# Performance work log

Measured on AMD Instinct MI355X. Metric: run time of the kernel, lower is better.

## Reference

```python
import jax, jax.numpy as jnp
import numpy as np

K = 7          # involution kernel size
GC = 16        # group_channels
BN_EPS = 1e-5


def conv1x1(x, w, b):
    # x: [b,c,h,w], w: [o,c], b: [o]
    return jnp.einsum('bchw,oc->bohw', x, w) + b[None, :, None, None]


def involution(x, w1, b1, w2, b2):
    # x: [b,c,h,w]; stride=1, kernel K, padding K//2
    b_, c, h, w = x.shape
    g = c // GC
    # per-pixel kernel weights: conv1x1 -> conv1x1 (no activation, as in source)
    wgt = conv1x1(conv1x1(x, w1, b1), w2, b2).reshape(b_, g, K * K, h, w)
    # patches: [b, c*K*K, h, w] with channel-major (c, kh, kw) ordering, matching torch Unfold
    pat = jax.lax.conv_general_dilated_patches(
        x, (K, K), (1, 1), ((K // 2, K // 2), (K // 2, K // 2)))
    pat = pat.reshape(b_, g, GC, K * K, h, w)
    out = jnp.einsum('bgkhw,bgckhw->bgchw', wgt, pat)
    return out.reshape(b_, c, h, w)


def hswish(x):
    return x * jnp.clip(x + 3.0, 0.0, 6.0) / 6.0


def setup_inputs() -> dict:
    key = jax.random.key(0)
    ks = jax.random.split(key, 20)
    inp, oup, mip = 256, 256, 64
    n, h, w = 16, 96, 96
    rr = 4  # involution reduction_ratio

    def rn(k, shape, s=0.05):
        return (jax.random.normal(k, shape) * s).astype(jnp.float32)

    def invp(k0, k1, k2, k3):
        return (rn(k0, (mip // rr, mip)), rn(k1, (mip // rr,)),
                rn(k2, (K * K * (mip // GC), mip // rr)),
                rn(k3, (K * K * (mip // GC),)))

    d = {}
    d['x'] = jax.random.normal(ks[0], (n, inp, h, w), dtype=jnp.float32)
    d['w_c1'] = rn(ks[1], (mip, inp)); d['b_c1'] = rn(ks[2], (mip,))
    d['inv1_w1'], d['inv1_b1'], d['inv1_w2'], d['inv1_b2'] = invp(ks[3], ks[4], ks[5], ks[6])
    d['bn_g'] = jnp.ones(mip, jnp.float32); d['bn_b'] = jnp.zeros(mip, jnp.float32)
    d['bn_m'] = jnp.zeros(mip, jnp.float32); d['bn_v'] = jnp.ones(mip, jnp.float32)
    d['invh_w1'], d['invh_b1'], d['invh_w2'], d['invh_b2'] = invp(ks[7], ks[8], ks[9], ks[10])
    d['w_h'] = rn(ks[11], (oup, mip)); d['b_h'] = rn(ks[12], (oup,))
    d['invw_w1'], d['invw_b1'], d['invw_w2'], d['invw_b2'] = invp(ks[13], ks[14], ks[15], ks[16])
    d['w_w'] = rn(ks[17], (oup, mip)); d['b_w'] = rn(ks[18], (oup,))
    return d


def reference(x, w_c1, b_c1, inv1_w1, inv1_b1, inv1_w2, inv1_b2,
              bn_g, bn_b, bn_m, bn_v,
              invh_w1, invh_b1, invh_w2, invh_b2, w_h, b_h,
              invw_w1, invw_b1, invw_w2, invw_b2, w_w, b_w):
    n, c, h, w = x.shape
    x_h = jnp.mean(x, axis=3, keepdims=True)                        # [n,c,h,1]
    x_w = jnp.mean(x, axis=2, keepdims=True).transpose(0, 1, 3, 2)  # [n,c,w,1]
    y = jnp.concatenate([x_h, x_w], axis=2)                          # [n,c,h+w,1]
    y = conv1x1(y, w_c1, b_c1)                                       # [n,mip,h+w,1]
    y = involution(y, inv1_w1, inv1_b1, inv1_w2, inv1_b2)
    inv_std = jax.lax.rsqrt(bn_v + BN_EPS)
    y = (y - bn_m[None, :, None, None]) * (bn_g * inv_std)[None, :, None, None] + bn_b[None, :, None, None]
    y = hswish(y)
    y_h = y[:, :, :h, :]                                             # [n,mip,h,1]
    y_w = y[:, :, h:, :].transpose(0, 1, 3, 2)                       # [n,mip,1,w]
    a_h = jax.nn.sigmoid(conv1x1(involution(y_h, invh_w1, invh_b1, invh_w2, invh_b2), w_h, b_h))
    a_w = jax.nn.sigmoid(conv1x1(involution(y_w, invw_w1, invw_b1, invw_w2, invw_b2), w_w, b_w))
    return x * a_w * a_h
```

## Files before the change

### kernel.cpp

```cpp
#include <hip/hip_runtime.h>
#include <math.h>

#define N_B   16
#define C_IN  256
#define MIP   64
#define HW    96
#define PTOT  192
#define KK    7

__global__ void prep_kernel(const float* __restrict__ w_h, const float* __restrict__ w_w,
                            float* __restrict__ wfT_h, float* __restrict__ wfT_w) {
    int idx = blockIdx.x * 256 + threadIdx.x;
    int sel = idx >> 14;
    int rem = idx & 16383;
    int co = rem >> 6;
    int ch = rem & 63;
    const float* src = sel ? w_w : w_h;
    float* dst = sel ? wfT_w : wfT_h;
    dst[ch * C_IN + co] = src[co * MIP + ch];
}

__global__ void pool_kernel(const float* __restrict__ x, float* __restrict__ pooled) {
    int plane = blockIdx.x;
    const float* xp = x + (size_t)plane * (HW * HW);
    __shared__ float sm[HW * 97];
    int t = threadIdx.x;
    #pragma unroll
    for (int k = 0; k < 9; ++k) {
        int idx = t + k * 256;
        float4 v = ((const float4*)xp)[idx];
        int flat = idx * 4;
        int row = flat / HW;
        int col = flat - row * HW;
        float* d = &sm[row * 97 + col];
        d[0] = v.x; d[1] = v.y; d[2] = v.z; d[3] = v.w;
    }
    __syncthreads();
    float* pp = pooled + (size_t)plane * PTOT;
    if (t < HW) {
        float rs = 0.f;
        #pragma unroll 4
        for (int j = 0; j < HW; ++j) rs += sm[t * 97 + j];
        pp[t] = rs * (1.f / 96.f);
    } else if (t < 2 * HW) {
        int c = t - HW;
        float cs = 0.f;
        #pragma unroll 4
        for (int i = 0; i < HW; ++i) cs += sm[i * 97 + c];
        pp[HW + c] = cs * (1.f / 96.f);
    }
}

__global__ void conv0_kernel(const float* __restrict__ pooled,
                             const float* __restrict__ w_c1, const float* __restrict__ b_c1,
                             float* __restrict__ y0) {
    int p0 = blockIdx.x * 16;
    int n  = blockIdx.y;
    int t  = threadIdx.x;
    __shared__ float pt[C_IN * 16];
    __shared__ float sw[64 * 65];
    const float* pn = pooled + (size_t)n * C_IN * PTOT;

    #pragma unroll
    for (int i = 0; i < 16; ++i) {
        int flat = t + 256 * i;
        int c = flat >> 4, pl = flat & 15;
        pt[flat] = pn[c * PTOT + p0 + pl];
    }

    int o = t & 63;
    int pl0 = (t >> 6) * 4;
    float acc0 = 0.f, acc1 = 0.f, acc2 = 0.f, acc3 = 0.f;

    for (int c0 = 0; c0 < C_IN; c0 += 64) {
        __syncthreads();
        #pragma unroll
        for (int i = 0; i < 16; ++i) {
            int flat = t + 256 * i;
            int oo = flat >> 6, cc = flat & 63;
            sw[oo * 65 + cc] = w_c1[oo * C_IN + c0 + cc];
        }
        __syncthreads();
        #pragma unroll 8
        for (int cc = 0; cc < 64; ++cc) {
            float wv = sw[o * 65 + cc];
            const float4 pv = *(const float4*)&pt[(c0 + cc) * 16 + pl0];
            acc0 += wv * pv.x;
            acc1 += wv * pv.y;
            acc2 += wv * pv.z;
            acc3 += wv * pv.w;
        }
    }
    float b = b_c1[o];
    size_t base = ((size_t)n * PTOT + p0 + pl0) * MIP + o;
    y0[base]            = acc0 + b;
    y0[base + MIP]      = acc1 + b;
    y0[base + 2 * MIP]  = acc2 + b;
    y0[base + 3 * MIP]  = acc3 + b;
}

__global__ void mid1_kernel(const float* __restrict__ y0,
                            const float* __restrict__ w1,   const float* __restrict__ b1,
                            const float* __restrict__ w2,   const float* __restrict__ b2,
                            const float* __restrict__ bn_g, const float* __restrict__ bn_b,
                            const float* __restrict__ bn_m, const float* __restrict__ bn_v,
                            float* __restrict__ y) {
    int p = blockIdx.x;
    int n = blockIdx.y;
    int t = threadIdx.x;
    __shared__ float ly0[KK][MIP];
    __shared__ float lt[16];
    __shared__ float lwgt[28];
    const float* yn = y0 + (size_t)n * PTOT * MIP;

    #pragma unroll
    for (int k = 0; k < KK; ++k) {
        int pp = p + k - 3;
        ly0[k][t] = (pp >= 0 && pp < PTOT) ? yn[pp * MIP + t] : 0.f;
    }
    __syncthreads();

    if (t < 16) {
        float acc = b1[t];
        const float* wr = w1 + t * MIP;
        #pragma unroll 8
        for (int o = 0; o < MIP; ++o) acc += wr[o] * ly0[3][o];
        lt[t] = acc;
    }
    __syncthreads();

    if (t < 28) {
        int g = t / KK, ky = t - g * KK;
        int q = g * 49 + ky * KK + 3;
        float acc = b2[q];
        const float* wr = w2 + q * 16;
        #pragma unroll
        for (int r = 0; r < 16; ++r) acc += wr[r] * lt[r];
        lwgt[t] = acc;
    }
    __syncthreads();

    {
        int g = t >> 4;
        float acc = 0.f;
        #pragma unroll
        for (int ky = 0; ky < KK; ++ky) acc += lwgt[g * KK + ky] * ly0[ky][t];
        float inv_std = rsqrtf(bn_v[t] + 1e-5f);
        float v = (acc - bn_m[t]) * (bn_g[t] * inv_std) + bn_b[t];
        float hs = v * fminf(fmaxf(v + 3.f, 0.f), 6.f) * (1.f / 6.f);
        y[((size_t)n * PTOT + p) * MIP + t] = hs;
    }
}

__global__ void mid2_kernel(const float* __restrict__ y,
                            const float* __restrict__ h_w1, const float* __restrict__ h_b1,
                            const float* __restrict__ h_w2, const float* __restrict__ h_b2,
                            const float* __restrict__ wfT_h, const float* __restrict__ b_h,
                            const float* __restrict__ v_w1, const float* __restrict__ v_b1,
                            const float* __restrict__ v_w2, const float* __restrict__ v_b2,
                            const float* __restrict__ wfT_w, const float* __restrict__ b_w,
                            float* __restrict__ a_h, float* __restrict__ a_w) {
    int p = blockIdx.x;
    int n = blockIdx.y;
    int t = threadIdx.x;
    int side = (p >= HW) ? 1 : 0;
    int pos = side ? (p - HW) : p;
    const float* w1 = side ? v_w1 : h_w1;
    const float* b1 = side ? v_b1 : h_b1;
    const float* w2 = side ? v_w2 : h_w2;
    const float* b2 = side ? v_b2 : h_b2;
    const float* wf = side ? wfT_w : wfT_h;
    const float* bf = side ? b_w : b_h;

    __shared__ float ly[KK][MIP];
    __shared__ float lt[16];
    __shared__ float lwgt[28];
    __shared__ float lz[MIP];
    const float* yn = y + (size_t)n * PTOT * MIP;

    #pragma unroll
    for (int k = 0; k < KK; ++k) {
        int q = pos + k - 3;
        float v = 0.f;
        if (q >= 0 && q < HW) v = yn[(side ? (HW + q) : q) * MIP + t];
        ly[k][t] = v;
    }
    __syncthreads();

    if (t < 16) {
        float acc = b1[t];
        const float* wr = w1 + t * MIP;
        #pragma unroll 8
        for (int o = 0; o < MIP; ++o) acc += wr[o] * ly[3][o];
        lt[t] = acc;
    }
    __syncthreads();

    if (t < 28) {
        int g = t / KK, kk = t - (t / KK) * KK;
        int q = side ? (g * 49 + 21 + kk) : (g * 49 + kk * KK + 3);
        float acc = b2[q];
        const float* wr = w2 + q * 16;
        #pragma unroll
        for (int r = 0; r < 16; ++r) acc += wr[r] * lt[r];
        lwgt[t] = acc;
    }
    __syncthreads();

    {
        int g = t >> 4;
        float acc = 0.f;
        #pragma unroll
        for (int k = 0; k < KK; ++k) acc += lwgt[g * KK + k] * ly[k][t];
        lz[t] = acc;
    }
    __syncthreads();

    float* dst = side ? a_w : a_h;
    #pragma unroll
    for (int q = 0; q < 4; ++q) {
        int co = q * 64 + t;
        float acc = bf[co];
        #pragma unroll 8
        for (int ch = 0; ch < MIP; ++ch) acc += wf[ch * C_IN + co] * lz[ch];
        float a = 1.f / (1.f + __expf(-acc));
        dst[((size_t)n * C_IN + co) * HW + pos] = a;
    }
}

__global__ void apply_kernel(const float* __restrict__ x,
                             const float* __restrict__ a_h, const float* __restrict__ a_w,
                             float* __restrict__ out) {
    int plane = blockIdx.x;
    const float4* xp = (const float4*)(x + (size_t)plane * (HW * HW));
    float4* op = (float4*)(out + (size_t)plane * (HW * HW));
    __shared__ float sah[HW];
    __shared__ float saw[HW];
    int t = threadIdx.x;
    if (t < HW) {
        sah[t] = a_h[(size_t)plane * HW + t];
        saw[t] = a_w[(size_t)plane * HW + t];
    }
    __syncthreads();
    #pragma unroll
    for (int k = 0; k < 9; ++k) {
        int idx = t + k * 256;
        float4 v = xp[idx];
        int row = idx / 24;
        int c4 = (idx - row * 24) * 4;
        float ah = sah[row];
        v.x *= ah * saw[c4 + 0];
        v.y *= ah * saw[c4 + 1];
        v.z *= ah * saw[c4 + 2];
        v.w *= ah * saw[c4 + 3];
        op[idx] = v;
    }
}

extern "C" void kernel_launch(void* const* d_in, const int* in_sizes, int n_in,
                              void* d_out, int out_size, void* d_ws, size_t ws_size,
                              hipStream_t stream) {
    const float* x      = (const float*)d_in[0];
    const float* w_c1   = (const float*)d_in[1];
    const float* b_c1   = (const float*)d_in[2];
    const float* i1_w1  = (const float*)d_in[3];
    const float* i1_b1  = (const float*)d_in[4];
    const float* i1_w2  = (const float*)d_in[5];
    const float* i1_b2  = (const float*)d_in[6];
    const float* bn_g   = (const float*)d_in[7];
    const float* bn_b   = (const float*)d_in[8];
    const float* bn_m   = (const float*)d_in[9];
    const float* bn_v   = (const float*)d_in[10];
    const float* ih_w1  = (const float*)d_in[11];
    const float* ih_b1  = (const float*)d_in[12];
    const float* ih_w2  = (const float*)d_in[13];
    const float* ih_b2  = (const float*)d_in[14];
    const float* w_h    = (const float*)d_in[15];
    const float* b_h    = (const float*)d_in[16];
    const float* iw_w1  = (const float*)d_in[17];
    const float* iw_b1  = (const float*)d_in[18];
    const float* iw_w2  = (const float*)d_in[19];
    const float* iw_b2  = (const float*)d_in[20];
    const float* w_w    = (const float*)d_in[21];
    const float* b_w    = (const float*)d_in[22];
    float* out = (float*)d_out;

    float* ws = (float*)d_ws;
    float* pooled = ws;
    float* y0     = pooled + 786432;
    float* y      = y0 + 196608;
    float* a_h    = y + 196608;
    float* a_w    = a_h + 393216;
    float* wfT_h  = a_w + 393216;
    float* wfT_w  = wfT_h + 16384;

    prep_kernel<<<dim3(128), dim3(256), 0, stream>>>(w_h, w_w, wfT_h, wfT_w);
    pool_kernel<<<dim3(N_B * C_IN), dim3(256), 0, stream>>>(x, pooled);
    conv0_kernel<<<dim3(12, N_B), dim3(256), 0, stream>>>(pooled, w_c1, b_c1, y0);
    mid1_kernel<<<dim3(PTOT, N_B), dim3(64), 0, stream>>>(
        y0, i1_w1, i1_b1, i1_w2, i1_b2, bn_g, bn_b, bn_m, bn_v, y);
    mid2_kernel<<<dim3(PTOT, N_B), dim3(64), 0, stream>>>(
        y, ih_w1, ih_b1, ih_w2, ih_b2, wfT_h, b_h,
        iw_w1, iw_b1, iw_w2, iw_b2, wfT_w, b_w, a_h, a_w);
    apply_kernel<<<dim3(N_B * C_IN), dim3(256), 0, stream>>>(x, a_h, a_w, out);
}
```

Before: 359.9 us.

## Fuse conv0, mid1 and mid2 into one tiled kernel with halo recompute

Merges the 1x1 conv, the first involution with BN and hswish, and both second-stage involutions plus final conv/sigmoid into a single kernel. Each block handles 16 positions and recomputes a 6-wide halo, so the y0 and y intermediates stay in shared memory instead of global, and the prep transpose kernel is dropped. The final conv is restructured to reuse each weight across 16 positions. The apply kernel now uses nontemporal stores. Only 192 blocks run the fused mid stage, and the halo adds redundant compute, which risks low GPU occupancy, but removing three launches should dominate in a pipeline that is mostly bandwidth-bound on pool and apply.

```diff
diff --git a/kernel.cpp b/kernel.cpp
--- a/kernel.cpp
+++ b/kernel.cpp
@@ -8,17 +8,7 @@
 #define PTOT  192
 #define KK    7
 
-__global__ void prep_kernel(const float* __restrict__ w_h, const float* __restrict__ w_w,
-                            float* __restrict__ wfT_h, float* __restrict__ wfT_w) {
-    int idx = blockIdx.x * 256 + threadIdx.x;
-    int sel = idx >> 14;
-    int rem = idx & 16383;
-    int co = rem >> 6;
-    int ch = rem & 63;
-    const float* src = sel ? w_w : w_h;
-    float* dst = sel ? wfT_w : wfT_h;
-    dst[ch * C_IN + co] = src[co * MIP + ch];
-}
+typedef float floatx4 __attribute__((ext_vector_type(4)));
 
 __global__ void pool_kernel(const float* __restrict__ x, float* __restrict__ pooled) {
     int plane = blockIdx.x;
@@ -28,7 +18,7 @@
     #pragma unroll
     for (int k = 0; k < 9; ++k) {
         int idx = t + k * 256;
-        float4 v = ((const float4*)xp)[idx];
+        floatx4 v = ((const floatx4*)xp)[idx];
         int flat = idx * 4;
         int row = flat / HW;
         int col = flat - row * HW;
@@ -51,26 +41,53 @@
     }
 }
 
-__global__ void conv0_kernel(const float* __restrict__ pooled,
-                             const float* __restrict__ w_c1, const float* __restrict__ b_c1,
-                             float* __restrict__ y0) {
+__global__ __launch_bounds__(256) void megamid_kernel(
+    const float* __restrict__ pooled,
+    const float* __restrict__ w_c1, const float* __restrict__ b_c1,
+    const float* __restrict__ i1_w1, const float* __restrict__ i1_b1,
+    const float* __restrict__ i1_w2, const float* __restrict__ i1_b2,
+    const float* __restrict__ bn_g, const float* __restrict__ bn_b,
+    const float* __restrict__ bn_m, const float* __restrict__ bn_v,
+    const float* __restrict__ h_w1, const float* __restrict__ h_b1,
+    const float* __restrict__ h_w2, const float* __restrict__ h_b2,
+    const float* __restrict__ w_h,  const float* __restrict__ b_h,
+    const float* __restrict__ v_w1, const float* __restrict__ v_b1,
+    const float* __restrict__ v_w2, const float* __restrict__ v_b2,
+    const float* __restrict__ w_w,  const float* __restrict__ b_w,
+    float* __restrict__ a_h, float* __restrict__ a_w)
+{
     int p0 = blockIdx.x * 16;
     int n  = blockIdx.y;
     int t  = threadIdx.x;
-    __shared__ float pt[C_IN * 16];
-    __shared__ float sw[64 * 65];
+    int side = (p0 >= HW) ? 1 : 0;
+    int lo = side * HW;
+
+    __shared__ float smem[15552];
+    float* pt   = smem;
+    float* sw   = smem + 8192;
+    float* y0t  = smem + 12352;
+    float* yt   = smem + 14144;
+    float* lt    = smem;
+    float* lwgt  = smem + 352;
+    float* lt2   = smem + 968;
+    float* lwgt2 = smem + 1224;
+    float* lz    = smem + 1672;
+
     const float* pn = pooled + (size_t)n * C_IN * PTOT;
 
     #pragma unroll
-    for (int i = 0; i < 16; ++i) {
+    for (int i = 0; i < 32; ++i) {
         int flat = t + 256 * i;
-        int c = flat >> 4, pl = flat & 15;
-        pt[flat] = pn[c * PTOT + p0 + pl];
+        int c = flat >> 5, j = flat & 31;
+        int r = p0 - 6 + j;
+        pt[flat] = (j < 28 && r >= 0 && r < PTOT) ? pn[c * PTOT + r] : 0.f;
     }
 
     int o = t & 63;
-    int pl0 = (t >> 6) * 4;
-    float acc0 = 0.f, acc1 = 0.f, acc2 = 0.f, acc3 = 0.f;
+    int j0 = (t >> 6) * 8;
+    float acc[8];
+    #pragma unroll
+    for (int e = 0; e < 8; ++e) acc[e] = 0.f;
 
     for (int c0 = 0; c0 < C_IN; c0 += 64) {
         __syncthreads();
@@ -81,150 +98,121 @@
             sw[oo * 65 + cc] = w_c1[oo * C_IN + c0 + cc];
         }
         __syncthreads();
-        #pragma unroll 8
+        #pragma unroll 4
         for (int cc = 0; cc < 64; ++cc) {
             float wv = sw[o * 65 + cc];
-            const float4 pv = *(const float4*)&pt[(c0 + cc) * 16 + pl0];
-            acc0 += wv * pv.x;
-            acc1 += wv * pv.y;
-            acc2 += wv * pv.z;
-            acc3 += wv * pv.w;
-        }
-    }
-    float b = b_c1[o];
-    size_t base = ((size_t)n * PTOT + p0 + pl0) * MIP + o;
-    y0[base]            = acc0 + b;
-    y0[base + MIP]      = acc1 + b;
-    y0[base + 2 * MIP]  = acc2 + b;
-    y0[base + 3 * MIP]  = acc3 + b;
-}
-
-__global__ void mid1_kernel(const float* __restrict__ y0,
-                            const float* __restrict__ w1,   const float* __restrict__ b1,
-                            const float* __restrict__ w2,   const float* __restrict__ b2,
-                            const float* __restrict__ bn_g, const float* __restrict__ bn_b,
-                            const float* __restrict__ bn_m, const float* __restrict__ bn_v,
-                            float* __restrict__ y) {
-    int p = blockIdx.x;
-    int n = blockIdx.y;
-    int t = threadIdx.x;
-    __shared__ float ly0[KK][MIP];
-    __shared__ float lt[16];
-    __shared__ float lwgt[28];
-    const float* yn = y0 + (size_t)n * PTOT * MIP;
-
-    #pragma unroll
-    for (int k = 0; k < KK; ++k) {
-        int pp = p + k - 3;
-        ly0[k][t] = (pp >= 0 && pp < PTOT) ? yn[pp * MIP + t] : 0.f;
-    }
-    __syncthreads();
-
-    if (t < 16) {
-        float acc = b1[t];
-        const float* wr = w1 + t * MIP;
+            const floatx4 pa = *(const floatx4*)&pt[(c0 + cc) * 32 + j0];
+            const floatx4 pb = *(const floatx4*)&pt[(c0 + cc) * 32 + j0 + 4];
+            acc[0] += wv * pa.x; acc[1] += wv * pa.y;
+            acc[2] += wv * pa.z; acc[3] += wv * pa.w;
+            acc[4] += wv * pb.x; acc[5] += wv * pb.y;
+            acc[6] += wv * pb.z; acc[7] += wv * pb.w;
+        }
+    }
+    {
+        float bo = b_c1[o];
+        #pragma unroll
+        for (int e = 0; e < 8; ++e) {
+            int j = j0 + e;
+            if (j < 28) {
+                int r = p0 - 6 + j;
+                y0t[j * 64 + o] = (r >= 0 && r < PTOT) ? (acc[e] + bo) : 0.f;
+            }
+        }
+    }
+    __syncthreads();
+
+    for (int idx = t; idx < 352; idx += 256) {
+        int q = idx >> 4, i = idx & 15;
+        float a = i1_b1[i];
+        const float* wr = i1_w1 + i * MIP;
         #pragma unroll 8
-        for (int o = 0; o < MIP; ++o) acc += wr[o] * ly0[3][o];
-        lt[t] = acc;
-    }
-    __syncthreads();
-
-    if (t < 28) {
-        int g = t / KK, ky = t - g * KK;
-        int q = g * 49 + ky * KK + 3;
-        float acc = b2[q];
-        const float* wr = w2 + q * 16;
-        #pragma unroll
-        for (int r = 0; r < 16; ++r) acc += wr[r] * lt[r];
-        lwgt[t] = acc;
-    }
-    __syncthreads();
+        for (int oo = 0; oo < MIP; ++oo) a += wr[oo] * y0t[(q + 3) * 64 + oo];
+        lt[idx] = a;
+    }
+    __syncthreads();
+    for (int idx = t; idx < 616; idx += 256) {
+        int q = idx / 28, m = idx - q * 28;
+        int g = m / 7, ky = m - g * 7;
+        int wq = g * 49 + ky * 7 + 3;
+        float a = i1_b2[wq];
+        const float* wr = i1_w2 + wq * 16;
+        #pragma unroll
+        for (int r = 0; r < 16; ++r) a += wr[r] * lt[q * 16 + r];
+        lwgt[idx] = a;
+    }
+    __syncthreads();
+    for (int idx = t; idx < 1408; idx += 256) {
+        int q = idx >> 6, ch = idx & 63;
+        int g = ch >> 4;
+        float a = 0.f;
+        #pragma unroll
+        for (int ky = 0; ky < KK; ++ky)
+            a += lwgt[q * 28 + g * 7 + ky] * y0t[(q + ky) * 64 + ch];
+        float inv_std = rsqrtf(bn_v[ch] + 1e-5f);
+        float v = (a - bn_m[ch]) * (bn_g[ch] * inv_std) + bn_b[ch];
+        yt[idx] = v * fminf(fmaxf(v + 3.f, 0.f), 6.f) * (1.f / 6.f);
+    }
+    __syncthreads();
+
+    const float* ww1 = side ? v_w1 : h_w1;
+    const float* bb1 = side ? v_b1 : h_b1;
+    const float* ww2 = side ? v_w2 : h_w2;
+    const float* bb2 = side ? v_b2 : h_b2;
+    const float* wf  = side ? w_w  : w_h;
+    const float* bf  = side ? b_w  : b_h;
 
     {
-        int g = t >> 4;
-        float acc = 0.f;
-        #pragma unroll
-        for (int ky = 0; ky < KK; ++ky) acc += lwgt[g * KK + ky] * ly0[ky][t];
-        float inv_std = rsqrtf(bn_v[t] + 1e-5f);
-        float v = (acc - bn_m[t]) * (bn_g[t] * inv_std) + bn_b[t];
-        float hs = v * fminf(fmaxf(v + 3.f, 0.f), 6.f) * (1.f / 6.f);
-        y[((size_t)n * PTOT + p) * MIP + t] = hs;
-    }
-}
-
-__global__ void mid2_kernel(const float* __restrict__ y,
-                            const float* __restrict__ h_w1, const float* __restrict__ h_b1,
-                            const float* __restrict__ h_w2, const float* __restrict__ h_b2,
-                            const float* __restrict__ wfT_h, const float* __restrict__ b_h,
-                            const float* __restrict__ v_w1, const float* __restrict__ v_b1,
-                            const float* __restrict__ v_w2, const float* __restrict__ v_b2,
-                            const float* __restrict__ wfT_w, const float* __restrict__ b_w,
-                            float* __restrict__ a_h, float* __restrict__ a_w) {
-    int p = blockIdx.x;
-    int n = blockIdx.y;
-    int t = threadIdx.x;
-    int side = (p >= HW) ? 1 : 0;
-    int pos = side ? (p - HW) : p;
-    const float* w1 = side ? v_w1 : h_w1;
-    const float* b1 = side ? v_b1 : h_b1;
-    const float* w2 = side ? v_w2 : h_w2;
-    const float* b2 = side ? v_b2 : h_b2;
-    const float* wf = side ? wfT_w : wfT_h;
-    const float* bf = side ? b_w : b_h;
-
-    __shared__ float ly[KK][MIP];
-    __shared__ float lt[16];
-    __shared__ float lwgt[28];
-    __shared__ float lz[MIP];
-    const float* yn = y + (size_t)n * PTOT * MIP;
-
-    #pragma unroll
-    for (int k = 0; k < KK; ++k) {
-        int q = pos + k - 3;
-        float v = 0.f;
-        if (q >= 0 && q < HW) v = yn[(side ? (HW + q) : q) * MIP + t];
-        ly[k][t] = v;
-    }
-    __syncthreads();
-
-    if (t < 16) {
-        float acc = b1[t];
-        const float* wr = w1 + t * MIP;
+        int pp = t >> 4, i = t & 15;
+        float a = bb1[i];
+        const float* wr = ww1 + i * MIP;
         #pragma unroll 8
-        for (int o = 0; o < MIP; ++o) acc += wr[o] * ly[3][o];
-        lt[t] = acc;
-    }
-    __syncthreads();
-
-    if (t < 28) {
-        int g = t / KK, kk = t - (t / KK) * KK;
-        int q = side ? (g * 49 + 21 + kk) : (g * 49 + kk * KK + 3);
-        float acc = b2[q];
-        const float* wr = w2 + q * 16;
-        #pragma unroll
-        for (int r = 0; r < 16; ++r) acc += wr[r] * lt[r];
-        lwgt[t] = acc;
-    }
-    __syncthreads();
-
+        for (int oo = 0; oo < MIP; ++oo) a += wr[oo] * yt[(pp + 3) * 64 + oo];
+        lt2[t] = a;
+    }
+    __syncthreads();
+    for (int idx = t; idx < 448; idx += 256) {
+        int pp = idx / 28, m = idx - pp * 28;
+        int g = m / 7, kk = m - g * 7;
+        int wq = side ? (g * 49 + 21 + kk) : (g * 49 + kk * 7 + 3);
+        float a = bb2[wq];
+        const float* wr = ww2 + wq * 16;
+        #pragma unroll
+        for (int r = 0; r < 16; ++r) a += wr[r] * lt2[pp * 16 + r];
+        lwgt2[idx] = a;
+    }
+    __syncthreads();
+    for (int idx = t; idx < 1024; idx += 256) {
+        int pp = idx >> 6, ch = idx & 63;
+        int g = ch >> 4;
+        float a = 0.f;
+        #pragma unroll
+        for (int k = 0; k < KK; ++k) {
+            int pos = p0 + pp + k - 3;
+            float v = (pos >= lo && pos < lo + HW) ? yt[(pp + k) * 64 + ch] : 0.f;
+            a += lwgt2[pp * 28 + g * 7 + k] * v;
+        }
+        lz[idx] = a;
+    }
+    __syncthreads();
     {
-        int g = t >> 4;
-        float acc = 0.f;
-        #pragma unroll
-        for (int k = 0; k < KK; ++k) acc += lwgt[g * KK + k] * ly[k][t];
-        lz[t] = acc;
-    }
-    __syncthreads();
-
-    float* dst = side ? a_w : a_h;
-    #pragma unroll
-    for (int q = 0; q < 4; ++q) {
-        int co = q * 64 + t;
-        float acc = bf[co];
-        #pragma unroll 8
-        for (int ch = 0; ch < MIP; ++ch) acc += wf[ch * C_IN + co] * lz[ch];
-        float a = 1.f / (1.f + __expf(-acc));
-        dst[((size_t)n * C_IN + co) * HW + pos] = a;
+        int co = t;
+        float accf[16];
+        float bfv = bf[co];
+        #pragma unroll
+        for (int pp = 0; pp < 16; ++pp) accf[pp] = bfv;
+        const float* wr = wf + co * MIP;
+        for (int ch = 0; ch < MIP; ++ch) {
+            float wv = wr[ch];
+            #pragma unroll
+            for (int pp = 0; pp < 16; ++pp)
+                accf[pp] += wv * lz[pp * 64 + ch];
+        }
+        float* dst = side ? a_w : a_h;
+        size_t basep = ((size_t)n * C_IN + co) * HW + (p0 - lo);
+        #pragma unroll
+        for (int pp = 0; pp < 16; ++pp)
+            dst[basep + pp] = 1.f / (1.f + __expf(-accf[pp]));
     }
 }
 
@@ -232,8 +220,8 @@
                              const float* __restrict__ a_h, const float* __restrict__ a_w,
                              float* __restrict__ out) {
     int plane = blockIdx.x;
-    const float4* xp = (const float4*)(x + (size_t)plane * (HW * HW));
-    float4* op = (float4*)(out + (size_t)plane * (HW * HW));
+    const floatx4* xp = (const floatx4*)(x + (size_t)plane * (HW * HW));
+    floatx4* op = (floatx4*)(out + (size_t)plane * (HW * HW));
     __shared__ float sah[HW];
     __shared__ float saw[HW];
     int t = threadIdx.x;
@@ -245,7 +233,7 @@
     #pragma unroll
     for (int k = 0; k < 9; ++k) {
         int idx = t + k * 256;
-        float4 v = xp[idx];
+        floatx4 v = xp[idx];
         int row = idx / 24;
         int c4 = (idx - row * 24) * 4;
         float ah = sah[row];
@@ -253,7 +241,7 @@
         v.y *= ah * saw[c4 + 1];
         v.z *= ah * saw[c4 + 2];
         v.w *= ah * saw[c4 + 3];
-        op[idx] = v;
+        __builtin_nontemporal_store(v, &op[idx]);
     }
 }
 
@@ -287,20 +275,14 @@
 
     float* ws = (float*)d_ws;
     float* pooled = ws;
-    float* y0     = pooled + 786432;
-    float* y      = y0 + 196608;
-    float* a_h    = y + 196608;
+    float* a_h    = pooled + 786432;
     float* a_w    = a_h + 393216;
-    float* wfT_h  = a_w + 393216;
-    float* wfT_w  = wfT_h + 16384;
-
-    prep_kernel<<<dim3(128), dim3(256), 0, stream>>>(w_h, w_w, wfT_h, wfT_w);
+
     pool_kernel<<<dim3(N_B * C_IN), dim3(256), 0, stream>>>(x, pooled);
-    conv0_kernel<<<dim3(12, N_B), dim3(256), 0, stream>>>(pooled, w_c1, b_c1, y0);
-    mid1_kernel<<<dim3(PTOT, N_B), dim3(64), 0, stream>>>(
-        y0, i1_w1, i1_b1, i1_w2, i1_b2, bn_g, bn_b, bn_m, bn_v, y);
-    mid2_kernel<<<dim3(PTOT, N_B), dim3(64), 0, stream>>>(
-        y, ih_w1, ih_b1, ih_w2, ih_b2, wfT_h, b_h,
-        iw_w1, iw_b1, iw_w2, iw_b2, wfT_w, b_w, a_h, a_w);
+    megamid_kernel<<<dim3(12, N_B), dim3(256), 0, stream>>>(
+        pooled, w_c1, b_c1, i1_w1, i1_b1, i1_w2, i1_b2,
+        bn_g, bn_b, bn_m, bn_v,
+        ih_w1, ih_b1, ih_w2, ih_b2, w_h, b_h,
+        iw_w1, iw_b1, iw_w2, iw_b2, w_w, b_w, a_h, a_w);
     apply_kernel<<<dim3(N_B * C_IN), dim3(256), 0, stream>>>(x, a_h, a_w, out);
 }
```

New measurement: 350.5 us. 1.03x faster.
